# Performance work log

Measured on AMD Instinct MI355X. Metric: run time of the kernel, lower is better.

The kernel has to match this reference:

```python
import jax, jax.numpy as jnp
import numpy as np

D_MODEL = 1024
NUM_HEADS = 16
HEAD_DIM = D_MODEL // NUM_HEADS
NUM_KERNELS = 21


def tisa_bias(amp, off, sharp, seq_len):
    # amp/off/sharp: (H, K). Returns (H, L, L) translation-invariant bias.
    # Evaluate on the 2L-1 distinct relative distances, then gather (Toeplitz).
    d = jnp.arange(-(seq_len - 1), seq_len, dtype=amp.dtype)  # (2L-1,)
    # (H, K, 2L-1) -> sum over kernels -> (H, 2L-1)
    scores = jnp.sum(
        amp[:, :, None]
        * jnp.exp(-jnp.abs(sharp)[:, :, None] * (d[None, None, :] - off[:, :, None]) ** 2),
        axis=1,
    )
    i = jnp.arange(seq_len)
    rel_idx = i[None, :] - i[:, None] + (seq_len - 1)  # (L, L) in [0, 2L-2]
    return scores[:, rel_idx]  # (H, L, L)


def setup_inputs() -> dict:
    key = jax.random.key(0)
    ks = jax.random.split(key, 9)
    B, L = 4, 1024
    s = 0.02
    return {
        "x_q": jax.random.normal(ks[0], (B, L, D_MODEL), dtype=jnp.float32),
        "x_kv": jax.random.normal(ks[1], (B, L, D_MODEL), dtype=jnp.float32),
        "Wq": jax.random.normal(ks[2], (D_MODEL, D_MODEL), dtype=jnp.float32) * s,
        "Wm": jax.random.normal(ks[3], (D_MODEL, 2 * D_MODEL), dtype=jnp.float32) * s,
        "Wg": jax.random.normal(ks[4], (D_MODEL, 2 * D_MODEL), dtype=jnp.float32) * s,
        "bg": jnp.zeros((2 * D_MODEL,), dtype=jnp.float32),
        "tisa_amp": jax.random.normal(ks[5], (NUM_HEADS, NUM_KERNELS), dtype=jnp.float32) * 0.1,
        "tisa_off": jax.random.uniform(ks[6], (NUM_HEADS, NUM_KERNELS), dtype=jnp.float32, minval=-512.0, maxval=512.0),
        "tisa_sharp": jax.random.uniform(ks[7], (NUM_HEADS, NUM_KERNELS), dtype=jnp.float32, minval=1e-4, maxval=0.05),
    }


def reference(x_q, x_kv, Wq, Wm, Wg, bg, tisa_amp, tisa_off, tisa_sharp):
    B, Lq, _ = x_q.shape
    Lkv = x_kv.shape[1]
    H, Dh = NUM_HEADS, HEAD_DIM

    q = (x_q @ Wq).reshape(B, Lq, H, Dh).transpose(0, 2, 1, 3)        # (B,H,Lq,Dh)
    mem = (x_kv @ Wm)                                                 # (B,Lkv,2D)
    k = mem[..., :D_MODEL].reshape(B, Lkv, H, Dh).transpose(0, 2, 1, 3)
    v = mem[..., D_MODEL:].reshape(B, Lkv, H, Dh).transpose(0, 2, 1, 3)

    scale = 1.0 / jnp.sqrt(jnp.asarray(Dh, dtype=q.dtype))
    scores = jnp.einsum("bhqd,bhkd->bhqk", q, k) * scale              # (B,H,Lq,Lkv)
    scores = scores + tisa_bias(tisa_amp, tisa_off, tisa_sharp, Lkv)[None]
    weights = jax.nn.softmax(scores, axis=-1)

    attn = jnp.einsum("bhqk,bhkd->bhqd", weights, v)                  # (B,H,Lq,Dh)
    attn = attn.transpose(0, 2, 1, 3).reshape(B, Lq, D_MODEL)

    g = attn @ Wg + bg                                                # (B,Lq,2D)
    a, b = g[..., :D_MODEL], g[..., D_MODEL:]
    return a * jax.nn.sigmoid(b)
```

## Files before the change

### kernel.cpp

```cpp
#include <hip/hip_runtime.h>
#include <cstdint>
#include <cstddef>

typedef __attribute__((ext_vector_type(8))) short bf16x8;
typedef __attribute__((ext_vector_type(4))) float f32x4;

#define LOG2E 1.44269504f

__device__ __forceinline__ unsigned short f2bf(float x) {
  unsigned int u = __float_as_uint(x);
  u += 0x7FFFu + ((u >> 16) & 1u);
  return (unsigned short)(u >> 16);
}
__device__ __forceinline__ unsigned short f2bf_trunc(float x) {
  return (unsigned short)(__float_as_uint(x) >> 16);
}

__device__ __forceinline__ void gload_lds16(const void* g, void* l) {
  __builtin_amdgcn_global_load_lds(
      (const __attribute__((address_space(1))) unsigned int*)g,
      (__attribute__((address_space(3))) unsigned int*)l, 16, 0, 0);
}


__global__ void preproc(const float* __restrict__ x_q, const float* __restrict__ x_kv,
                        const float* __restrict__ Wq, const float* __restrict__ Wm,
                        const float* __restrict__ Wg,
                        const float* __restrict__ amp, const float* __restrict__ off,
                        const float* __restrict__ sharp,
                        ushort4* __restrict__ bXq, ushort4* __restrict__ bXkv,
                        unsigned short* __restrict__ dWq, unsigned short* __restrict__ dWm,
                        unsigned short* __restrict__ dWg, float* __restrict__ tab) {
  __shared__ float tile[32][33];
  const int blk = blockIdx.x;
  if (blk < 8192) {
    int i = blk * 256 + threadIdx.x;
    float4 v;
    ushort4* d;
    if (i < (1 << 20)) { v = ((const float4*)x_q)[i]; d = bXq + i; }
    else { int j = i - (1 << 20); v = ((const float4*)x_kv)[j]; d = bXkv + j; }
    ushort4 o;
    o.x = f2bf(v.x); o.y = f2bf(v.y); o.z = f2bf(v.z); o.w = f2bf(v.w);
    *d = o;
  } else if (blk < 14336) {
    int idx = blk - 8192;
    int z = idx >> 11, rem = idx & 2047;
    int bx = rem & 63, by = rem >> 6;
    const float* src = z == 0 ? Wq : (z == 1 ? Wm : Wg);
    unsigned short* dst = z == 0 ? dWq : (z == 1 ? dWm : dWg);
    int N = z == 0 ? 1024 : 2048;
    int nb = bx * 32, kb = by * 32;
    if (nb >= N) return;
    int tx = threadIdx.x & 31, ty = threadIdx.x >> 5;
#pragma unroll
    for (int r = ty; r < 32; r += 8)
      tile[r][tx] = src[(size_t)(kb + r) * N + nb + tx];
    __syncthreads();
#pragma unroll
    for (int r = ty; r < 32; r += 8)
      dst[(size_t)(nb + r) * 1024 + kb + tx] = f2bf(tile[tx][r]);
  } else {
    int h = blk - 14336;
    for (int idx = threadIdx.x; idx < 2047; idx += 256) {
      float d = (float)(idx - 1023);
      float acc = 0.f;
#pragma unroll
      for (int k = 0; k < 21; ++k) {
        float dd = d - off[h * 21 + k];
        acc += amp[h * 21 + k] * __expf(-fabsf(sharp[h * 21 + k]) * dd * dd);
      }
      tab[h * 2047 + idx] = acc * LOG2E;
    }
  }
}


__global__ __launch_bounds__(256)
void qkv_gemm(const unsigned short* __restrict__ Xq,
              const unsigned short* __restrict__ Xkv,
              const unsigned short* __restrict__ WqT,
              const unsigned short* __restrict__ WmT,
              unsigned short* __restrict__ qbuf,
              unsigned short* __restrict__ kbuf,
              unsigned short* __restrict__ vtbuf) {
  __shared__ unsigned short sA[2][128 * 32];
  __shared__ unsigned short sB[2][128 * 32];
  const int bx = blockIdx.x;
  const bool isQ = bx < 8;
  const int ntile = (isQ ? bx : bx - 8) << 7;
  const unsigned short* A = isQ ? Xq : Xkv;
  const unsigned short* B = (isQ ? WqT : WmT) + (size_t)ntile * 1024;
  const int t = threadIdx.x, lane = t & 63, w = t >> 6;
  const int wm = (w >> 1) << 6, wn = (w & 1) << 6;
  const int mtile = blockIdx.y << 7;
  const int c = lane & 15, g = lane >> 4;
  const int srow = t >> 2, scol = (t & 3) << 3;
  const unsigned short* aP = A + (size_t)(mtile + srow) * 1024 + scol;
  const unsigned short* bP = B + (size_t)srow * 1024 + scol;
  const int lo = srow * 32 + scol;

  gload_lds16(aP, &sA[0][lo]);
  gload_lds16(aP + 64 * 1024, &sA[0][lo + 64 * 32]);
  gload_lds16(bP, &sB[0][lo]);
  gload_lds16(bP + 64 * 1024, &sB[0][lo + 64 * 32]);
  __syncthreads();

  f32x4 acc[4][4] = {};
  for (int kt = 0; kt < 32; ++kt) {
    const int cur = kt & 1;
    if (kt + 1 < 32) {
      const int ko = (kt + 1) * 32;
      gload_lds16(aP + ko, &sA[1 - cur][lo]);
      gload_lds16(aP + 64 * 1024 + ko, &sA[1 - cur][lo + 64 * 32]);
      gload_lds16(bP + ko, &sB[1 - cur][lo]);
      gload_lds16(bP + 64 * 1024 + ko, &sB[1 - cur][lo + 64 * 32]);
    }
    bf16x8 af[4], bfr[4];
#pragma unroll
    for (int i = 0; i < 4; ++i) {
      af[i]  = *(const bf16x8*)&sA[cur][(wm + i * 16 + c) * 32 + g * 8];
      bfr[i] = *(const bf16x8*)&sB[cur][(wn + i * 16 + c) * 32 + g * 8];
    }
#pragma unroll
    for (int i = 0; i < 4; ++i)
#pragma unroll
      for (int j = 0; j < 4; ++j)
        acc[i][j] = __builtin_amdgcn_mfma_f32_16x16x32_bf16(af[i], bfr[j], acc[i][j], 0, 0, 0);
    __syncthreads();
  }

  const int row0 = mtile + wm + (g << 2);
  const int col0 = ntile + wn + c;
  if (isQ) {
#pragma unroll
    for (int i = 0; i < 4; ++i)
#pragma unroll
      for (int j = 0; j < 4; ++j) {
        int r = row0 + i * 16, cl = col0 + j * 16;
#pragma unroll
        for (int ri = 0; ri < 4; ++ri)
          qbuf[(size_t)(r + ri) * 1024 + cl] = f2bf(acc[i][j][ri] * (0.125f * LOG2E));
      }
  } else {
#pragma unroll
    for (int i = 0; i < 4; ++i)
#pragma unroll
      for (int j = 0; j < 4; ++j) {
        int r = row0 + i * 16, cl = col0 + j * 16;
        if (cl < 1024) {
#pragma unroll
          for (int ri = 0; ri < 4; ++ri)
            kbuf[(size_t)(r + ri) * 1024 + cl] = f2bf(acc[i][j][ri]);
        } else {
          int d = cl - 1024;
          int hh = d >> 6, dh = d & 63;
          int bb = r >> 10, ll = r & 1023;
          ushort4 pk;
          pk.x = f2bf(acc[i][j][0]);
          pk.y = f2bf(acc[i][j][1]);
          pk.z = f2bf(acc[i][j][2]);
          pk.w = f2bf(acc[i][j][3]);
          *(ushort4*)&vtbuf[((size_t)((bb * 16 + hh) * 64 + dh) << 10) + ll] = pk;
        }
      }
  }
}


__global__ __launch_bounds__(512, 4)
void attn_kernel(const unsigned short* __restrict__ qbuf,
                 const unsigned short* __restrict__ kbuf,
                 const unsigned short* __restrict__ vtbuf,
                 const float* __restrict__ biasTab,
                 unsigned short* __restrict__ attnb) {
  const int h = blockIdx.x & 15, b = blockIdx.x >> 4, qt = blockIdx.y;
  __shared__ unsigned short sK[2][64 * 64];
  __shared__ unsigned short sV[2][64 * 64];
  __shared__ unsigned short sQP[128 * 64];
  __shared__ float sLsum[2][128];
  const int t = threadIdx.x, lane = t & 63, w = t >> 6;
  const int c = lane & 15, g = lane >> 4;
  const int rg = w >> 1, cg = w & 1;

  const int r = t >> 3, ch = (t & 7) ^ (r & 7);

  const unsigned short* qsrc = qbuf + (size_t)(b * 1024 + qt * 128) * 1024 + h * 64;
  const unsigned short* ksrc = kbuf + (size_t)(b * 1024) * 1024 + h * 64;
  const unsigned short* vsrc = vtbuf + (size_t)((b * 16 + h) * 64) * 1024;

  gload_lds16(qsrc + (size_t)r * 1024 + ch * 8, &sQP[t * 8]);
  gload_lds16(qsrc + (size_t)(r + 64) * 1024 + ch * 8, &sQP[4096 + t * 8]);
  gload_lds16(ksrc + (size_t)r * 1024 + ch * 8, &sK[0][t * 8]);
  gload_lds16(vsrc + (size_t)r * 1024 + ch * 8, &sV[0][t * 8]);
  __syncthreads();

  bf16x8 aq[2][2];
#pragma unroll
  for (int rf = 0; rf < 2; ++rf) {
    int row = rg * 32 + rf * 16 + c;
#pragma unroll
    for (int ks = 0; ks < 2; ++ks)
      aq[rf][ks] = *(const bf16x8*)&sQP[row * 64 + (((ks * 4 + g) ^ (row & 7)) * 8)];
  }
  __syncthreads();

  f32x4 o[2][2] = {};
  float lsum[2][4] = {};
  const float* bb = biasTab + h * 2047 + 1023 + cg * 32 + c - qt * 128 - rg * 32 - g * 4;

  for (int kv = 0; kv < 16; ++kv) {
    const int cur = kv & 1;

    const float* bk = bb + kv * 64;
    f32x4 s[2][2];
#pragma unroll
    for (int rf = 0; rf < 2; ++rf)
#pragma unroll
      for (int nf = 0; nf < 2; ++nf)
#pragma unroll
        for (int ri = 0; ri < 4; ++ri)
          s[rf][nf][ri] = bk[(nf - rf) * 16 - ri];

    if (kv + 1 < 16) {
      gload_lds16(ksrc + (size_t)((kv + 1) * 64 + r) * 1024 + ch * 8, &sK[1 - cur][t * 8]);
      gload_lds16(vsrc + (size_t)r * 1024 + (kv + 1) * 64 + ch * 8, &sV[1 - cur][t * 8]);
    }

#pragma unroll
    for (int nf = 0; nf < 2; ++nf) {
      int krow = cg * 32 + nf * 16 + c;
      bf16x8 b0 = *(const bf16x8*)&sK[cur][krow * 64 + (((g) ^ (krow & 7)) * 8)];
      bf16x8 b1 = *(const bf16x8*)&sK[cur][krow * 64 + (((4 + g) ^ (krow & 7)) * 8)];
#pragma unroll
      for (int rf = 0; rf < 2; ++rf) {
        s[rf][nf] = __builtin_amdgcn_mfma_f32_16x16x32_bf16(aq[rf][0], b0, s[rf][nf], 0, 0, 0);
        s[rf][nf] = __builtin_amdgcn_mfma_f32_16x16x32_bf16(aq[rf][1], b1, s[rf][nf], 0, 0, 0);
      }
    }

#pragma unroll
    for (int rf = 0; rf < 2; ++rf)
#pragma unroll
      for (int nf = 0; nf < 2; ++nf)
#pragma unroll
        for (int ri = 0; ri < 4; ++ri) {
          float e = exp2f(s[rf][nf][ri]);
          lsum[rf][ri] += e;
          int prow = rg * 32 + rf * 16 + g * 4 + ri;
          int chunk = cg * 4 + nf * 2 + (c >> 3);
          sQP[prow * 64 + ((chunk ^ (prow & 7)) * 8) + (c & 7)] = f2bf_trunc(e);
        }
    __syncthreads();

    bf16x8 ap[2][2];
#pragma unroll
    for (int rf = 0; rf < 2; ++rf) {
      int row = rg * 32 + rf * 16 + c;
#pragma unroll
      for (int ks = 0; ks < 2; ++ks)
        ap[rf][ks] = *(const bf16x8*)&sQP[row * 64 + (((ks * 4 + g) ^ (row & 7)) * 8)];
    }
#pragma unroll
    for (int df = 0; df < 2; ++df) {
      int vrow = cg * 32 + df * 16 + c;
      bf16x8 b0 = *(const bf16x8*)&sV[cur][vrow * 64 + (((g) ^ (vrow & 7)) * 8)];
      bf16x8 b1 = *(const bf16x8*)&sV[cur][vrow * 64 + (((4 + g) ^ (vrow & 7)) * 8)];
#pragma unroll
      for (int rf = 0; rf < 2; ++rf) {
        o[rf][df] = __builtin_amdgcn_mfma_f32_16x16x32_bf16(ap[rf][0], b0, o[rf][df], 0, 0, 0);
        o[rf][df] = __builtin_amdgcn_mfma_f32_16x16x32_bf16(ap[rf][1], b1, o[rf][df], 0, 0, 0);
      }
    }
    __syncthreads();
  }

#pragma unroll
  for (int off = 1; off < 16; off <<= 1)
#pragma unroll
    for (int rf = 0; rf < 2; ++rf)
#pragma unroll
      for (int ri = 0; ri < 4; ++ri)
        lsum[rf][ri] += __shfl_xor(lsum[rf][ri], off, 64);
  if (c == 0) {
#pragma unroll
    for (int rf = 0; rf < 2; ++rf)
#pragma unroll
      for (int ri = 0; ri < 4; ++ri)
        sLsum[cg][rg * 32 + rf * 16 + g * 4 + ri] = lsum[rf][ri];
  }
  __syncthreads();

  unsigned short* obase = attnb +
      (size_t)(b * 1024 + qt * 128 + rg * 32 + g * 4) * 1024 + h * 64 + cg * 32 + c;
#pragma unroll
  for (int rf = 0; rf < 2; ++rf)
#pragma unroll
    for (int ri = 0; ri < 4; ++ri) {
      int row = rg * 32 + rf * 16 + g * 4 + ri;
      float rinv = 1.0f / (sLsum[0][row] + sLsum[1][row]);
#pragma unroll
      for (int df = 0; df < 2; ++df)
        obase[(size_t)(rf * 16 + ri) * 1024 + df * 16] = f2bf(o[rf][df][ri] * rinv);
    }
}


__global__ __launch_bounds__(256)
void out_gemm(const unsigned short* __restrict__ A,
              const unsigned short* __restrict__ WgT,
              const float* __restrict__ bg,
              float* __restrict__ out) {
  __shared__ unsigned short sA[2][128 * 32];
  __shared__ unsigned short sB[2][128 * 32];
  const int nb = blockIdx.x;
  const int mtile = blockIdx.y << 7;
  const int t = threadIdx.x, lane = t & 63, w = t >> 6;
  const int c = lane & 15, g = lane >> 4;
  const int srow = t >> 2, scol = (t & 3) << 3;
  const unsigned short* aP = A + (size_t)(mtile + srow) * 1024 + scol;
  const unsigned short* bP0 = WgT + (size_t)(nb * 64 + srow) * 1024 + scol;
  const unsigned short* bP1 = WgT + (size_t)(1024 + nb * 64 + srow) * 1024 + scol;
  const int lo = srow * 32 + scol;

  gload_lds16(aP, &sA[0][lo]);
  gload_lds16(aP + 64 * 1024, &sA[0][lo + 64 * 32]);
  gload_lds16(bP0, &sB[0][lo]);
  gload_lds16(bP1, &sB[0][lo + 64 * 32]);
  __syncthreads();

  f32x4 acc[2][8] = {};
  for (int kt = 0; kt < 32; ++kt) {
    const int cur = kt & 1;
    if (kt + 1 < 32) {
      const int ko = (kt + 1) * 32;
      gload_lds16(aP + ko, &sA[1 - cur][lo]);
      gload_lds16(aP + 64 * 1024 + ko, &sA[1 - cur][lo + 64 * 32]);
      gload_lds16(bP0 + ko, &sB[1 - cur][lo]);
      gload_lds16(bP1 + ko, &sB[1 - cur][lo + 64 * 32]);
    }
    bf16x8 af[2], bfr[8];
#pragma unroll
    for (int i = 0; i < 2; ++i)
      af[i] = *(const bf16x8*)&sA[cur][(w * 32 + i * 16 + c) * 32 + g * 8];
#pragma unroll
    for (int j = 0; j < 8; ++j)
      bfr[j] = *(const bf16x8*)&sB[cur][(j * 16 + c) * 32 + g * 8];
#pragma unroll
    for (int i = 0; i < 2; ++i)
#pragma unroll
      for (int j = 0; j < 8; ++j)
        acc[i][j] = __builtin_amdgcn_mfma_f32_16x16x32_bf16(af[i], bfr[j], acc[i][j], 0, 0, 0);
    __syncthreads();
  }

#pragma unroll
  for (int i = 0; i < 2; ++i) {
    int row0 = mtile + w * 32 + i * 16 + (g << 2);
#pragma unroll
    for (int jj = 0; jj < 4; ++jj) {
      int col = nb * 64 + jj * 16 + c;
      float ba = bg[col];
      float bbv = bg[1024 + col];
#pragma unroll
      for (int ri = 0; ri < 4; ++ri) {
        float av = acc[i][jj][ri] + ba;
        float bv = acc[i][jj + 4][ri] + bbv;
        out[(size_t)(row0 + ri) * 1024 + col] = av / (1.f + exp2f(-LOG2E * bv));
      }
    }
  }
}


extern "C" void kernel_launch(void* const* d_in, const int* in_sizes, int n_in,
                              void* d_out, int out_size, void* d_ws, size_t ws_size,
                              hipStream_t stream) {
  const float* x_q   = (const float*)d_in[0];
  const float* x_kv  = (const float*)d_in[1];
  const float* Wq    = (const float*)d_in[2];
  const float* Wm    = (const float*)d_in[3];
  const float* Wg    = (const float*)d_in[4];
  const float* bg    = (const float*)d_in[5];
  const float* amp   = (const float*)d_in[6];
  const float* off   = (const float*)d_in[7];
  const float* sharp = (const float*)d_in[8];
  float* out = (float*)d_out;

  char* ws = (char*)d_ws;
  size_t o = 0;
  auto alloc = [&](size_t bytes) {
    char* p = ws + o;
    o += (bytes + 255) & ~(size_t)255;
    return p;
  };
  unsigned short* bXq   = (unsigned short*)alloc(4096ull * 1024 * 2);
  unsigned short* bXkv  = (unsigned short*)alloc(4096ull * 1024 * 2);
  unsigned short* bWqT  = (unsigned short*)alloc(1024ull * 1024 * 2);
  unsigned short* bWmT  = (unsigned short*)alloc(2048ull * 1024 * 2);
  unsigned short* bWgT  = (unsigned short*)alloc(2048ull * 1024 * 2);
  float*          biasT = (float*)alloc(16ull * 2047 * 4);
  unsigned short* qbuf  = (unsigned short*)alloc(4096ull * 1024 * 2);
  unsigned short* kbuf  = (unsigned short*)alloc(4096ull * 1024 * 2);
  unsigned short* vtbuf = (unsigned short*)alloc(4096ull * 1024 * 2);
  unsigned short* attnb = (unsigned short*)alloc(4096ull * 1024 * 2);
  if (ws_size < o) return;

  preproc<<<14352, 256, 0, stream>>>(x_q, x_kv, Wq, Wm, Wg, amp, off, sharp,
                                     (ushort4*)bXq, (ushort4*)bXkv,
                                     bWqT, bWmT, bWgT, biasT);
  qkv_gemm<<<dim3(24, 32), 256, 0, stream>>>(bXq, bXkv, bWqT, bWmT, qbuf, kbuf, vtbuf);
  attn_kernel<<<dim3(64, 8), 512, 0, stream>>>(qbuf, kbuf, vtbuf, biasT, attnb);
  out_gemm<<<dim3(16, 32), 256, 0, stream>>>(attnb, bWgT, bg, out);
}
```

Baseline: 217.6 us.

## Give each attention wave full kv columns, halve out_gemm M tile

The attention kernel drops from 512 to 256 threads. Each wave now owns 32 query rows across all 64 kv columns and all 64 head dims, with a private P buffer in shared memory. This removes the per-iteration barrier between the P write and read, and the shared-memory row-sum reduction at the end, at the cost of more accumulator registers per thread. The output GEMM tile shrinks from 128 to 64 rows, doubling the grid to spread work over more CUs, and qkv_gemm/out_gemm get a min-blocks occupancy hint.

```diff
diff --git a/kernel.cpp b/kernel.cpp
--- a/kernel.cpp
+++ b/kernel.cpp
@@ -75,7 +75,7 @@
 }
 
 
-__global__ __launch_bounds__(256)
+__global__ __launch_bounds__(256, 4)
 void qkv_gemm(const unsigned short* __restrict__ Xq,
               const unsigned short* __restrict__ Xkv,
               const unsigned short* __restrict__ WqT,
@@ -167,7 +167,7 @@
 }
 
 
-__global__ __launch_bounds__(512, 4)
+__global__ __launch_bounds__(256)
 void attn_kernel(const unsigned short* __restrict__ qbuf,
                  const unsigned short* __restrict__ kbuf,
                  const unsigned short* __restrict__ vtbuf,
@@ -176,99 +176,111 @@
   const int h = blockIdx.x & 15, b = blockIdx.x >> 4, qt = blockIdx.y;
   __shared__ unsigned short sK[2][64 * 64];
   __shared__ unsigned short sV[2][64 * 64];
-  __shared__ unsigned short sQP[128 * 64];
-  __shared__ float sLsum[2][128];
+  __shared__ unsigned short sP[4][32 * 64];
   const int t = threadIdx.x, lane = t & 63, w = t >> 6;
   const int c = lane & 15, g = lane >> 4;
-  const int rg = w >> 1, cg = w & 1;
-
-  const int r = t >> 3, ch = (t & 7) ^ (r & 7);
+
+  const int r8 = t >> 3, pc = t & 7;
 
   const unsigned short* qsrc = qbuf + (size_t)(b * 1024 + qt * 128) * 1024 + h * 64;
   const unsigned short* ksrc = kbuf + (size_t)(b * 1024) * 1024 + h * 64;
   const unsigned short* vsrc = vtbuf + (size_t)((b * 16 + h) * 64) * 1024;
 
-  gload_lds16(qsrc + (size_t)r * 1024 + ch * 8, &sQP[t * 8]);
-  gload_lds16(qsrc + (size_t)(r + 64) * 1024 + ch * 8, &sQP[4096 + t * 8]);
-  gload_lds16(ksrc + (size_t)r * 1024 + ch * 8, &sK[0][t * 8]);
-  gload_lds16(vsrc + (size_t)r * 1024 + ch * 8, &sV[0][t * 8]);
+  unsigned short* sQ = &sP[0][0];
+#pragma unroll
+  for (int q = 0; q < 4; ++q) {
+    int row = q * 32 + r8;
+    gload_lds16(qsrc + (size_t)row * 1024 + (pc ^ (row & 7)) * 8, &sQ[q * 2048 + t * 8]);
+  }
+#pragma unroll
+  for (int u = 0; u < 2; ++u) {
+    int row = u * 32 + r8;
+    int ch = pc ^ (row & 7);
+    gload_lds16(ksrc + (size_t)row * 1024 + ch * 8, &sK[0][u * 2048 + t * 8]);
+    gload_lds16(vsrc + (size_t)row * 1024 + ch * 8, &sV[0][u * 2048 + t * 8]);
+  }
   __syncthreads();
 
   bf16x8 aq[2][2];
 #pragma unroll
   for (int rf = 0; rf < 2; ++rf) {
-    int row = rg * 32 + rf * 16 + c;
+    int row = w * 32 + rf * 16 + c;
 #pragma unroll
     for (int ks = 0; ks < 2; ++ks)
-      aq[rf][ks] = *(const bf16x8*)&sQP[row * 64 + (((ks * 4 + g) ^ (row & 7)) * 8)];
-  }
-  __syncthreads();
-
-  f32x4 o[2][2] = {};
+      aq[rf][ks] = *(const bf16x8*)&sQ[row * 64 + (((ks * 4 + g) ^ (row & 7)) * 8)];
+  }
+
+  f32x4 o[2][4] = {};
   float lsum[2][4] = {};
-  const float* bb = biasTab + h * 2047 + 1023 + cg * 32 + c - qt * 128 - rg * 32 - g * 4;
+  const float* b0 = biasTab + h * 2047 + 1023 + c - qt * 128 - w * 32 - g * 4;
 
   for (int kv = 0; kv < 16; ++kv) {
     const int cur = kv & 1;
 
-    const float* bk = bb + kv * 64;
-    f32x4 s[2][2];
+    f32x4 s[2][4];
+    const float* bk = b0 + kv * 64;
 #pragma unroll
     for (int rf = 0; rf < 2; ++rf)
 #pragma unroll
-      for (int nf = 0; nf < 2; ++nf)
+      for (int nf = 0; nf < 4; ++nf)
 #pragma unroll
         for (int ri = 0; ri < 4; ++ri)
           s[rf][nf][ri] = bk[(nf - rf) * 16 - ri];
 
     if (kv + 1 < 16) {
-      gload_lds16(ksrc + (size_t)((kv + 1) * 64 + r) * 1024 + ch * 8, &sK[1 - cur][t * 8]);
-      gload_lds16(vsrc + (size_t)r * 1024 + (kv + 1) * 64 + ch * 8, &sV[1 - cur][t * 8]);
-    }
-
-#pragma unroll
-    for (int nf = 0; nf < 2; ++nf) {
-      int krow = cg * 32 + nf * 16 + c;
-      bf16x8 b0 = *(const bf16x8*)&sK[cur][krow * 64 + (((g) ^ (krow & 7)) * 8)];
-      bf16x8 b1 = *(const bf16x8*)&sK[cur][krow * 64 + (((4 + g) ^ (krow & 7)) * 8)];
+#pragma unroll
+      for (int u = 0; u < 2; ++u) {
+        int row = u * 32 + r8;
+        int ch = pc ^ (row & 7);
+        gload_lds16(ksrc + (size_t)((kv + 1) * 64 + row) * 1024 + ch * 8,
+                    &sK[1 - cur][u * 2048 + t * 8]);
+        gload_lds16(vsrc + (size_t)row * 1024 + (kv + 1) * 64 + ch * 8,
+                    &sV[1 - cur][u * 2048 + t * 8]);
+      }
+    }
+
+#pragma unroll
+    for (int nf = 0; nf < 4; ++nf) {
+      int krow = nf * 16 + c;
+      bf16x8 k0 = *(const bf16x8*)&sK[cur][krow * 64 + (((g) ^ (krow & 7)) * 8)];
+      bf16x8 k1 = *(const bf16x8*)&sK[cur][krow * 64 + (((4 + g) ^ (krow & 7)) * 8)];
 #pragma unroll
       for (int rf = 0; rf < 2; ++rf) {
-        s[rf][nf] = __builtin_amdgcn_mfma_f32_16x16x32_bf16(aq[rf][0], b0, s[rf][nf], 0, 0, 0);
-        s[rf][nf] = __builtin_amdgcn_mfma_f32_16x16x32_bf16(aq[rf][1], b1, s[rf][nf], 0, 0, 0);
+        s[rf][nf] = __builtin_amdgcn_mfma_f32_16x16x32_bf16(aq[rf][0], k0, s[rf][nf], 0, 0, 0);
+        s[rf][nf] = __builtin_amdgcn_mfma_f32_16x16x32_bf16(aq[rf][1], k1, s[rf][nf], 0, 0, 0);
       }
     }
 
 #pragma unroll
     for (int rf = 0; rf < 2; ++rf)
 #pragma unroll
-      for (int nf = 0; nf < 2; ++nf)
+      for (int nf = 0; nf < 4; ++nf)
 #pragma unroll
         for (int ri = 0; ri < 4; ++ri) {
           float e = exp2f(s[rf][nf][ri]);
           lsum[rf][ri] += e;
-          int prow = rg * 32 + rf * 16 + g * 4 + ri;
-          int chunk = cg * 4 + nf * 2 + (c >> 3);
-          sQP[prow * 64 + ((chunk ^ (prow & 7)) * 8) + (c & 7)] = f2bf_trunc(e);
+          int prow = rf * 16 + g * 4 + ri;
+          sP[w][prow * 64 + (((nf * 2 + (c >> 3)) ^ (prow & 7)) * 8) + (c & 7)] = f2bf_trunc(e);
         }
-    __syncthreads();
 
     bf16x8 ap[2][2];
 #pragma unroll
     for (int rf = 0; rf < 2; ++rf) {
-      int row = rg * 32 + rf * 16 + c;
+      int prow = rf * 16 + c;
 #pragma unroll
       for (int ks = 0; ks < 2; ++ks)
-        ap[rf][ks] = *(const bf16x8*)&sQP[row * 64 + (((ks * 4 + g) ^ (row & 7)) * 8)];
-    }
-#pragma unroll
-    for (int df = 0; df < 2; ++df) {
-      int vrow = cg * 32 + df * 16 + c;
-      bf16x8 b0 = *(const bf16x8*)&sV[cur][vrow * 64 + (((g) ^ (vrow & 7)) * 8)];
-      bf16x8 b1 = *(const bf16x8*)&sV[cur][vrow * 64 + (((4 + g) ^ (vrow & 7)) * 8)];
+        ap[rf][ks] = *(const bf16x8*)&sP[w][prow * 64 + (((ks * 4 + g) ^ (prow & 7)) * 8)];
+    }
+
+#pragma unroll
+    for (int df = 0; df < 4; ++df) {
+      int vrow = df * 16 + c;
+      bf16x8 v0 = *(const bf16x8*)&sV[cur][vrow * 64 + (((g) ^ (vrow & 7)) * 8)];
+      bf16x8 v1 = *(const bf16x8*)&sV[cur][vrow * 64 + (((4 + g) ^ (vrow & 7)) * 8)];
 #pragma unroll
       for (int rf = 0; rf < 2; ++rf) {
-        o[rf][df] = __builtin_amdgcn_mfma_f32_16x16x32_bf16(ap[rf][0], b0, o[rf][df], 0, 0, 0);
-        o[rf][df] = __builtin_amdgcn_mfma_f32_16x16x32_bf16(ap[rf][1], b1, o[rf][df], 0, 0, 0);
+        o[rf][df] = __builtin_amdgcn_mfma_f32_16x16x32_bf16(ap[rf][0], v0, o[rf][df], 0, 0, 0);
+        o[rf][df] = __builtin_amdgcn_mfma_f32_16x16x32_bf16(ap[rf][1], v1, o[rf][df], 0, 0, 0);
       }
     }
     __syncthreads();
@@ -281,41 +293,33 @@
 #pragma unroll
       for (int ri = 0; ri < 4; ++ri)
         lsum[rf][ri] += __shfl_xor(lsum[rf][ri], off, 64);
-  if (c == 0) {
-#pragma unroll
-    for (int rf = 0; rf < 2; ++rf)
-#pragma unroll
-      for (int ri = 0; ri < 4; ++ri)
-        sLsum[cg][rg * 32 + rf * 16 + g * 4 + ri] = lsum[rf][ri];
-  }
-  __syncthreads();
-
-  unsigned short* obase = attnb +
-      (size_t)(b * 1024 + qt * 128 + rg * 32 + g * 4) * 1024 + h * 64 + cg * 32 + c;
+
+  unsigned short* ob = attnb + (size_t)(b * 1024 + qt * 128 + w * 32) * 1024 + h * 64;
 #pragma unroll
   for (int rf = 0; rf < 2; ++rf)
 #pragma unroll
     for (int ri = 0; ri < 4; ++ri) {
-      int row = rg * 32 + rf * 16 + g * 4 + ri;
-      float rinv = 1.0f / (sLsum[0][row] + sLsum[1][row]);
-#pragma unroll
-      for (int df = 0; df < 2; ++df)
-        obase[(size_t)(rf * 16 + ri) * 1024 + df * 16] = f2bf(o[rf][df][ri] * rinv);
-    }
-}
-
-
-__global__ __launch_bounds__(256)
+      float rinv = 1.0f / lsum[rf][ri];
+      size_t rowoff = (size_t)(rf * 16 + g * 4 + ri) * 1024;
+#pragma unroll
+      for (int df = 0; df < 4; ++df)
+        ob[rowoff + df * 16 + c] = f2bf(o[rf][df][ri] * rinv);
+    }
+}
+
+
+__global__ __launch_bounds__(256, 4)
 void out_gemm(const unsigned short* __restrict__ A,
               const unsigned short* __restrict__ WgT,
               const float* __restrict__ bg,
               float* __restrict__ out) {
-  __shared__ unsigned short sA[2][128 * 32];
+  __shared__ unsigned short sA[2][64 * 32];
   __shared__ unsigned short sB[2][128 * 32];
   const int nb = blockIdx.x;
-  const int mtile = blockIdx.y << 7;
+  const int mtile = blockIdx.y << 6;
   const int t = threadIdx.x, lane = t & 63, w = t >> 6;
   const int c = lane & 15, g = lane >> 4;
+  const int rm = w >> 1, cn = w & 1;
   const int srow = t >> 2, scol = (t & 3) << 3;
   const unsigned short* aP = A + (size_t)(mtile + srow) * 1024 + scol;
   const unsigned short* bP0 = WgT + (size_t)(nb * 64 + srow) * 1024 + scol;
@@ -323,48 +327,48 @@
   const int lo = srow * 32 + scol;
 
   gload_lds16(aP, &sA[0][lo]);
-  gload_lds16(aP + 64 * 1024, &sA[0][lo + 64 * 32]);
   gload_lds16(bP0, &sB[0][lo]);
   gload_lds16(bP1, &sB[0][lo + 64 * 32]);
   __syncthreads();
 
-  f32x4 acc[2][8] = {};
+  f32x4 acc[2][4] = {};
   for (int kt = 0; kt < 32; ++kt) {
     const int cur = kt & 1;
     if (kt + 1 < 32) {
       const int ko = (kt + 1) * 32;
       gload_lds16(aP + ko, &sA[1 - cur][lo]);
-      gload_lds16(aP + 64 * 1024 + ko, &sA[1 - cur][lo + 64 * 32]);
       gload_lds16(bP0 + ko, &sB[1 - cur][lo]);
       gload_lds16(bP1 + ko, &sB[1 - cur][lo + 64 * 32]);
     }
-    bf16x8 af[2], bfr[8];
+    bf16x8 af[2], bfr[4];
 #pragma unroll
     for (int i = 0; i < 2; ++i)
-      af[i] = *(const bf16x8*)&sA[cur][(w * 32 + i * 16 + c) * 32 + g * 8];
-#pragma unroll
-    for (int j = 0; j < 8; ++j)
-      bfr[j] = *(const bf16x8*)&sB[cur][(j * 16 + c) * 32 + g * 8];
+      af[i] = *(const bf16x8*)&sA[cur][(rm * 32 + i * 16 + c) * 32 + g * 8];
+#pragma unroll
+    for (int jj = 0; jj < 2; ++jj) {
+      bfr[jj]     = *(const bf16x8*)&sB[cur][(cn * 32 + jj * 16 + c) * 32 + g * 8];
+      bfr[jj + 2] = *(const bf16x8*)&sB[cur][(64 + cn * 32 + jj * 16 + c) * 32 + g * 8];
+    }
 #pragma unroll
     for (int i = 0; i < 2; ++i)
 #pragma unroll
-      for (int j = 0; j < 8; ++j)
+      for (int j = 0; j < 4; ++j)
         acc[i][j] = __builtin_amdgcn_mfma_f32_16x16x32_bf16(af[i], bfr[j], acc[i][j], 0, 0, 0);
     __syncthreads();
   }
 
 #pragma unroll
   for (int i = 0; i < 2; ++i) {
-    int row0 = mtile + w * 32 + i * 16 + (g << 2);
-#pragma unroll
-    for (int jj = 0; jj < 4; ++jj) {
-      int col = nb * 64 + jj * 16 + c;
+    int row0 = mtile + rm * 32 + i * 16 + (g << 2);
+#pragma unroll
+    for (int jj = 0; jj < 2; ++jj) {
+      int col = nb * 64 + cn * 32 + jj * 16 + c;
       float ba = bg[col];
       float bbv = bg[1024 + col];
 #pragma unroll
       for (int ri = 0; ri < 4; ++ri) {
         float av = acc[i][jj][ri] + ba;
-        float bv = acc[i][jj + 4][ri] + bbv;
+        float bv = acc[i][jj + 2][ri] + bbv;
         out[(size_t)(row0 + ri) * 1024 + col] = av / (1.f + exp2f(-LOG2E * bv));
       }
     }
@@ -409,6 +413,6 @@
                                      (ushort4*)bXq, (ushort4*)bXkv,
                                      bWqT, bWmT, bWgT, biasT);
   qkv_gemm<<<dim3(24, 32), 256, 0, stream>>>(bXq, bXkv, bWqT, bWmT, qbuf, kbuf, vtbuf);
-  attn_kernel<<<dim3(64, 8), 512, 0, stream>>>(qbuf, kbuf, vtbuf, biasT, attnb);
-  out_gemm<<<dim3(16, 32), 256, 0, stream>>>(attnb, bWgT, bg, out);
-}
+  attn_kernel<<<dim3(64, 8), 256, 0, stream>>>(qbuf, kbuf, vtbuf, biasT, attnb);
+  out_gemm<<<dim3(16, 64), 256, 0, stream>>>(attnb, bWgT, bg, out);
+}
```

Measured after the change: 232.7 us. 1.07x slower.

## Drop per-iteration attention barrier via extra P/V buffers; shrink out_gemm tile

Applied to the files above, without the earlier changes.

In the attention loop, P now has two LDS buffers and V has three rotating buffers. This lets the barrier at the end of each KV iteration be removed, leaving one barrier per iteration. The output GEMM now uses 64-row M tiles with a 2x2 wave layout, which doubles its grid, and both GEMMs get a min-blocks launch-bounds hint. In exchange, attention LDS use roughly doubles, which may limit co-resident blocks, and the smaller GEMM tiles reuse each loaded operand less.

```diff
diff --git a/kernel.cpp b/kernel.cpp
--- a/kernel.cpp
+++ b/kernel.cpp
@@ -75,7 +75,7 @@
 }
 
 
-__global__ __launch_bounds__(256)
+__global__ __launch_bounds__(256, 4)
 void qkv_gemm(const unsigned short* __restrict__ Xq,
               const unsigned short* __restrict__ Xkv,
               const unsigned short* __restrict__ WqT,
@@ -167,7 +167,7 @@
 }
 
 
-__global__ __launch_bounds__(512, 4)
+__global__ __launch_bounds__(512)
 void attn_kernel(const unsigned short* __restrict__ qbuf,
                  const unsigned short* __restrict__ kbuf,
                  const unsigned short* __restrict__ vtbuf,
@@ -175,8 +175,8 @@
                  unsigned short* __restrict__ attnb) {
   const int h = blockIdx.x & 15, b = blockIdx.x >> 4, qt = blockIdx.y;
   __shared__ unsigned short sK[2][64 * 64];
-  __shared__ unsigned short sV[2][64 * 64];
-  __shared__ unsigned short sQP[128 * 64];
+  __shared__ unsigned short sV[3][64 * 64];
+  __shared__ unsigned short sP[2][128 * 64];
   __shared__ float sLsum[2][128];
   const int t = threadIdx.x, lane = t & 63, w = t >> 6;
   const int c = lane & 15, g = lane >> 4;
@@ -188,8 +188,9 @@
   const unsigned short* ksrc = kbuf + (size_t)(b * 1024) * 1024 + h * 64;
   const unsigned short* vsrc = vtbuf + (size_t)((b * 16 + h) * 64) * 1024;
 
-  gload_lds16(qsrc + (size_t)r * 1024 + ch * 8, &sQP[t * 8]);
-  gload_lds16(qsrc + (size_t)(r + 64) * 1024 + ch * 8, &sQP[4096 + t * 8]);
+  unsigned short* sQ = &sP[0][0];
+  gload_lds16(qsrc + (size_t)r * 1024 + ch * 8, &sQ[t * 8]);
+  gload_lds16(qsrc + (size_t)(r + 64) * 1024 + ch * 8, &sQ[4096 + t * 8]);
   gload_lds16(ksrc + (size_t)r * 1024 + ch * 8, &sK[0][t * 8]);
   gload_lds16(vsrc + (size_t)r * 1024 + ch * 8, &sV[0][t * 8]);
   __syncthreads();
@@ -200,7 +201,7 @@
     int row = rg * 32 + rf * 16 + c;
 #pragma unroll
     for (int ks = 0; ks < 2; ++ks)
-      aq[rf][ks] = *(const bf16x8*)&sQP[row * 64 + (((ks * 4 + g) ^ (row & 7)) * 8)];
+      aq[rf][ks] = *(const bf16x8*)&sQ[row * 64 + (((ks * 4 + g) ^ (row & 7)) * 8)];
   }
   __syncthreads();
 
@@ -208,6 +209,7 @@
   float lsum[2][4] = {};
   const float* bb = biasTab + h * 2047 + 1023 + cg * 32 + c - qt * 128 - rg * 32 - g * 4;
 
+  int vcur = 0, vnx = 1;
   for (int kv = 0; kv < 16; ++kv) {
     const int cur = kv & 1;
 
@@ -223,18 +225,18 @@
 
     if (kv + 1 < 16) {
       gload_lds16(ksrc + (size_t)((kv + 1) * 64 + r) * 1024 + ch * 8, &sK[1 - cur][t * 8]);
-      gload_lds16(vsrc + (size_t)r * 1024 + (kv + 1) * 64 + ch * 8, &sV[1 - cur][t * 8]);
+      gload_lds16(vsrc + (size_t)r * 1024 + (kv + 1) * 64 + ch * 8, &sV[vnx][t * 8]);
     }
 
 #pragma unroll
     for (int nf = 0; nf < 2; ++nf) {
       int krow = cg * 32 + nf * 16 + c;
-      bf16x8 b0 = *(const bf16x8*)&sK[cur][krow * 64 + (((g) ^ (krow & 7)) * 8)];
-      bf16x8 b1 = *(const bf16x8*)&sK[cur][krow * 64 + (((4 + g) ^ (krow & 7)) * 8)];
+      bf16x8 k0 = *(const bf16x8*)&sK[cur][krow * 64 + (((g) ^ (krow & 7)) * 8)];
+      bf16x8 k1 = *(const bf16x8*)&sK[cur][krow * 64 + (((4 + g) ^ (krow & 7)) * 8)];
 #pragma unroll
       for (int rf = 0; rf < 2; ++rf) {
-        s[rf][nf] = __builtin_amdgcn_mfma_f32_16x16x32_bf16(aq[rf][0], b0, s[rf][nf], 0, 0, 0);
-        s[rf][nf] = __builtin_amdgcn_mfma_f32_16x16x32_bf16(aq[rf][1], b1, s[rf][nf], 0, 0, 0);
+        s[rf][nf] = __builtin_amdgcn_mfma_f32_16x16x32_bf16(aq[rf][0], k0, s[rf][nf], 0, 0, 0);
+        s[rf][nf] = __builtin_amdgcn_mfma_f32_16x16x32_bf16(aq[rf][1], k1, s[rf][nf], 0, 0, 0);
       }
     }
 
@@ -248,7 +250,7 @@
           lsum[rf][ri] += e;
           int prow = rg * 32 + rf * 16 + g * 4 + ri;
           int chunk = cg * 4 + nf * 2 + (c >> 3);
-          sQP[prow * 64 + ((chunk ^ (prow & 7)) * 8) + (c & 7)] = f2bf_trunc(e);
+          sP[cur][prow * 64 + ((chunk ^ (prow & 7)) * 8) + (c & 7)] = f2bf_trunc(e);
         }
     __syncthreads();
 
@@ -258,20 +260,21 @@
       int row = rg * 32 + rf * 16 + c;
 #pragma unroll
       for (int ks = 0; ks < 2; ++ks)
-        ap[rf][ks] = *(const bf16x8*)&sQP[row * 64 + (((ks * 4 + g) ^ (row & 7)) * 8)];
+        ap[rf][ks] = *(const bf16x8*)&sP[cur][row * 64 + (((ks * 4 + g) ^ (row & 7)) * 8)];
     }
 #pragma unroll
     for (int df = 0; df < 2; ++df) {
       int vrow = cg * 32 + df * 16 + c;
-      bf16x8 b0 = *(const bf16x8*)&sV[cur][vrow * 64 + (((g) ^ (vrow & 7)) * 8)];
-      bf16x8 b1 = *(const bf16x8*)&sV[cur][vrow * 64 + (((4 + g) ^ (vrow & 7)) * 8)];
+      bf16x8 v0 = *(const bf16x8*)&sV[vcur][vrow * 64 + (((g) ^ (vrow & 7)) * 8)];
+      bf16x8 v1 = *(const bf16x8*)&sV[vcur][vrow * 64 + (((4 + g) ^ (vrow & 7)) * 8)];
 #pragma unroll
       for (int rf = 0; rf < 2; ++rf) {
-        o[rf][df] = __builtin_amdgcn_mfma_f32_16x16x32_bf16(ap[rf][0], b0, o[rf][df], 0, 0, 0);
-        o[rf][df] = __builtin_amdgcn_mfma_f32_16x16x32_bf16(ap[rf][1], b1, o[rf][df], 0, 0, 0);
-      }
-    }
-    __syncthreads();
+        o[rf][df] = __builtin_amdgcn_mfma_f32_16x16x32_bf16(ap[rf][0], v0, o[rf][df], 0, 0, 0);
+        o[rf][df] = __builtin_amdgcn_mfma_f32_16x16x32_bf16(ap[rf][1], v1, o[rf][df], 0, 0, 0);
+      }
+    }
+    vcur = vnx;
+    vnx = (vnx == 2) ? 0 : vnx + 1;
   }
 
 #pragma unroll
@@ -305,17 +308,18 @@
 }
 
 
-__global__ __launch_bounds__(256)
+__global__ __launch_bounds__(256, 4)
 void out_gemm(const unsigned short* __restrict__ A,
               const unsigned short* __restrict__ WgT,
               const float* __restrict__ bg,
               float* __restrict__ out) {
-  __shared__ unsigned short sA[2][128 * 32];
+  __shared__ unsigned short sA[2][64 * 32];
   __shared__ unsigned short sB[2][128 * 32];
   const int nb = blockIdx.x;
-  const int mtile = blockIdx.y << 7;
+  const int mtile = blockIdx.y << 6;
   const int t = threadIdx.x, lane = t & 63, w = t >> 6;
   const int c = lane & 15, g = lane >> 4;
+  const int rm = w >> 1, cn = w & 1;
   const int srow = t >> 2, scol = (t & 3) << 3;
   const unsigned short* aP = A + (size_t)(mtile + srow) * 1024 + scol;
   const unsigned short* bP0 = WgT + (size_t)(nb * 64 + srow) * 1024 + scol;
@@ -323,48 +327,48 @@
   const int lo = srow * 32 + scol;
 
   gload_lds16(aP, &sA[0][lo]);
-  gload_lds16(aP + 64 * 1024, &sA[0][lo + 64 * 32]);
   gload_lds16(bP0, &sB[0][lo]);
   gload_lds16(bP1, &sB[0][lo + 64 * 32]);
   __syncthreads();
 
-  f32x4 acc[2][8] = {};
+  f32x4 acc[2][4] = {};
   for (int kt = 0; kt < 32; ++kt) {
     const int cur = kt & 1;
     if (kt + 1 < 32) {
       const int ko = (kt + 1) * 32;
       gload_lds16(aP + ko, &sA[1 - cur][lo]);
-      gload_lds16(aP + 64 * 1024 + ko, &sA[1 - cur][lo + 64 * 32]);
       gload_lds16(bP0 + ko, &sB[1 - cur][lo]);
       gload_lds16(bP1 + ko, &sB[1 - cur][lo + 64 * 32]);
     }
-    bf16x8 af[2], bfr[8];
+    bf16x8 af[2], bfr[4];
 #pragma unroll
     for (int i = 0; i < 2; ++i)
-      af[i] = *(const bf16x8*)&sA[cur][(w * 32 + i * 16 + c) * 32 + g * 8];
-#pragma unroll
-    for (int j = 0; j < 8; ++j)
-      bfr[j] = *(const bf16x8*)&sB[cur][(j * 16 + c) * 32 + g * 8];
+      af[i] = *(const bf16x8*)&sA[cur][(rm * 32 + i * 16 + c) * 32 + g * 8];
+#pragma unroll
+    for (int jj = 0; jj < 2; ++jj) {
+      bfr[jj]     = *(const bf16x8*)&sB[cur][(cn * 32 + jj * 16 + c) * 32 + g * 8];
+      bfr[jj + 2] = *(const bf16x8*)&sB[cur][(64 + cn * 32 + jj * 16 + c) * 32 + g * 8];
+    }
 #pragma unroll
     for (int i = 0; i < 2; ++i)
 #pragma unroll
-      for (int j = 0; j < 8; ++j)
+      for (int j = 0; j < 4; ++j)
         acc[i][j] = __builtin_amdgcn_mfma_f32_16x16x32_bf16(af[i], bfr[j], acc[i][j], 0, 0, 0);
     __syncthreads();
   }
 
 #pragma unroll
   for (int i = 0; i < 2; ++i) {
-    int row0 = mtile + w * 32 + i * 16 + (g << 2);
-#pragma unroll
-    for (int jj = 0; jj < 4; ++jj) {
-      int col = nb * 64 + jj * 16 + c;
+    int row0 = mtile + rm * 32 + i * 16 + (g << 2);
+#pragma unroll
+    for (int jj = 0; jj < 2; ++jj) {
+      int col = nb * 64 + cn * 32 + jj * 16 + c;
       float ba = bg[col];
       float bbv = bg[1024 + col];
 #pragma unroll
       for (int ri = 0; ri < 4; ++ri) {
         float av = acc[i][jj][ri] + ba;
-        float bv = acc[i][jj + 4][ri] + bbv;
+        float bv = acc[i][jj + 2][ri] + bbv;
         out[(size_t)(row0 + ri) * 1024 + col] = av / (1.f + exp2f(-LOG2E * bv));
       }
     }
@@ -410,5 +414,5 @@
                                      bWqT, bWmT, bWgT, biasT);
   qkv_gemm<<<dim3(24, 32), 256, 0, stream>>>(bXq, bXkv, bWqT, bWmT, qbuf, kbuf, vtbuf);
   attn_kernel<<<dim3(64, 8), 512, 0, stream>>>(qbuf, kbuf, vtbuf, biasT, attnb);
-  out_gemm<<<dim3(16, 32), 256, 0, stream>>>(attnb, bWgT, bg, out);
-}
+  out_gemm<<<dim3(16, 64), 256, 0, stream>>>(attnb, bWgT, bg, out);
+}
```

New measurement: 209.0 us. 1.04x faster.
